# Kernel optimization log

Hardware: AMD Instinct MI355X
Metric: run time of the kernel (lower is better)

The kernel has to match this reference:

```python
import jax, jax.numpy as jnp
import numpy as np

N_NODES = 50000
N_EDGES = 1600000
NODE_DIM = 64
EDGE_DIM = 32
UNITS = 64


def _glorot(key, shape):
    fan_in, fan_out = shape[0], shape[1]
    lim = jnp.sqrt(6.0 / (fan_in + fan_out))
    return jax.random.uniform(key, shape, jnp.float32, -lim, lim)


def setup_inputs() -> dict:
    key = jax.random.key(0)
    ks = jax.random.split(key, 16)
    msg_in = 2 * NODE_DIM + EDGE_DIM  # concat(sender, receiver, edge)
    upd_in = NODE_DIM + UNITS         # concat(node, aggregated)
    return {
        "node_features": jax.random.normal(ks[0], (N_NODES, NODE_DIM), jnp.float32),
        "edge_features": jax.random.normal(ks[1], (N_EDGES, EDGE_DIM), jnp.float32),
        "senders": jax.random.randint(ks[2], (N_EDGES,), 0, N_NODES, jnp.int32),
        "receivers": jnp.sort(jax.random.randint(ks[3], (N_EDGES,), 0, N_NODES, jnp.int32)),
        # message_net
        "W1": _glorot(ks[4], (msg_in, UNITS)), "b1": jnp.zeros((UNITS,), jnp.float32),
        "W2": _glorot(ks[5], (UNITS, UNITS)), "b2": jnp.zeros((UNITS,), jnp.float32),
        # attention_net
        "Wa1": _glorot(ks[6], (msg_in, UNITS)), "ba1": jnp.zeros((UNITS,), jnp.float32),
        "Wa2": _glorot(ks[7], (UNITS, 1)), "ba2": jnp.zeros((1,), jnp.float32),
        # update_net
        "Wu1": _glorot(ks[8], (upd_in, UNITS)), "bu1": jnp.zeros((UNITS,), jnp.float32),
        "Wu2": _glorot(ks[9], (UNITS, UNITS)), "bu2": jnp.zeros((UNITS,), jnp.float32),
    }


def reference(node_features, edge_features, senders, receivers,
              W1, b1, W2, b2, Wa1, ba1, Wa2, ba2, Wu1, bu1, Wu2, bu2):
    act = jax.nn.swish
    # gather + concat: [E, 2*node_dim + edge_dim]
    msg_in = jnp.concatenate(
        [node_features[senders], node_features[receivers], edge_features], axis=-1)
    # message MLP
    messages = act(msg_in @ W1 + b1) @ W2 + b2  # [E, units]
    # attention: softmax over ALL edges (axis=0), as in the original
    att_logits = act(msg_in @ Wa1 + ba1) @ Wa2 + ba2  # [E, 1]
    att = jax.nn.softmax(att_logits, axis=0)
    messages = messages * att
    # scatter-sum to receivers
    aggregated = jax.ops.segment_sum(messages, receivers, num_segments=node_features.shape[0])
    upd_in = jnp.concatenate([node_features, aggregated], axis=-1)
    return act(upd_in @ Wu1 + bu1) @ Wu2 + bu2  # [N, units]
```

## Files before the change

### kernel.cpp

```cpp
#include <hip/hip_runtime.h>
#include <cstdint>
#include <cstddef>

#define N_NODES_C 50000
#define N_EDGES_C 1600000

typedef __attribute__((ext_vector_type(8)))  short bf16x8;
typedef __attribute__((ext_vector_type(16))) float f32x16;
typedef unsigned short ushort_t;

static const size_t AGG_OFF   = 256;
static const size_t NB_OFF    = 256 + (size_t)N_NODES_C * 64 * 4;
static const size_t WIMG_OFF  = NB_OFF + (size_t)N_NODES_C * 64 * 2;
static const size_t WUIMG_OFF = WIMG_OFF + 52224;

__device__ __forceinline__ float swish_(float v) { return v / (1.0f + __expf(-v)); }

__device__ __forceinline__ unsigned short f2bf(float f) {
    unsigned int u = __float_as_uint(f);
    return (unsigned short)((u + 0x7FFFu + ((u >> 16) & 1u)) >> 16);
}
__device__ __forceinline__ unsigned int pack2(float a, float b) {
    return (unsigned int)f2bf(a) | ((unsigned int)f2bf(b) << 16);
}

typedef __attribute__((address_space(3))) unsigned int lds_u32_t;
typedef const __attribute__((address_space(1))) unsigned int glb_u32_t;
__device__ __forceinline__ void glds16(const void* g, void* l) {
    __builtin_amdgcn_global_load_lds((glb_u32_t*)g, (lds_u32_t*)l, 16, 0, 0);
}

__global__ __launch_bounds__(256) void k_prep_node(const float* __restrict__ node,
                                                   ushort_t* __restrict__ node_bf)
{
    int i = blockIdx.x * 256 + threadIdx.x;
    if (i >= N_NODES_C * 64 / 8) return;
    const float4* s = (const float4*)node + (size_t)i * 2;
    float4 a = s[0], b = s[1];
    uint4 p = { pack2(a.x,a.y), pack2(a.z,a.w), pack2(b.x,b.y), pack2(b.z,b.w) };
    ((uint4*)node_bf)[i] = p;
}

__global__ __launch_bounds__(256) void k_prep_w(
    const float* __restrict__ W1, const float* __restrict__ Wa1,
    const float* __restrict__ W2, const float* __restrict__ Wu1,
    const float* __restrict__ Wu2,
    ushort_t* __restrict__ wm, ushort_t* __restrict__ wa, ushort_t* __restrict__ w2t,
    ushort_t* __restrict__ wu1t, ushort_t* __restrict__ wu2t)
{
    int b = blockIdx.x, t = threadIdx.x;
    const float* W; ushort_t* dst; int K, LP, p;
    if (b < 21)      { W = W1;  dst = wm;   K = 160; LP = 84; p = b * 256 + t; }
    else if (b < 42) { W = Wa1; dst = wa;   K = 160; LP = 84; p = (b-21)*256 + t; }
    else if (b < 51) { W = W2;  dst = w2t;  K = 64;  LP = 36; p = (b-42)*256 + t; }
    else if (b < 68) { W = Wu1; dst = wu1t; K = 128; LP = 68; p = (b-51)*256 + t; }
    else             { W = Wu2; dst = wu2t; K = 64;  LP = 36; p = (b-68)*256 + t; }
    int n = p / LP; int k2 = (p - n * LP) * 2;
    if (n >= 64) return;
    float a = (k2     < K) ? W[(size_t)k2 * 64 + n]       : 0.f;
    float c = (k2 + 1 < K) ? W[(size_t)(k2 + 1) * 64 + n] : 0.f;
    *(unsigned int*)(dst + (size_t)n * LP * 2 + k2) = pack2(a, c);
}

__global__ __launch_bounds__(512, 2) void k_edge(
    const ushort_t* __restrict__ node_bf, const float* __restrict__ edgef,
    const int* __restrict__ senders, const int* __restrict__ receivers,
    const ushort_t* __restrict__ wimg,
    const float* __restrict__ b1, const float* __restrict__ ba1,
    const float* __restrict__ Wa2, const float* __restrict__ ba2,
    const float* __restrict__ b2,
    float* __restrict__ expsum, float* __restrict__ agg)
{
    __shared__ ushort_t As[256 * 64];
    __shared__ ushort_t Ar[256 * 64];
    __shared__ ushort_t Ae[256 * 32];
    __shared__ ushort_t WmWa[21504];
    __shared__ ushort_t W2s[64 * 72];
    __shared__ float psum[8];

    const int tid = threadIdx.x;
    const int e0 = blockIdx.x * 256;

    for (int c = tid; c < 2688; c += 512)
        glds16((const char*)wimg + c * 16, (char*)WmWa + c * 16);
    for (int c = tid; c < 576; c += 512)
        glds16((const char*)wimg + 43008 + c * 16, (char*)W2s + c * 16);
    #pragma unroll
    for (int i = 0; i < 4; ++i) {
        int cg = tid + i * 512;
        int row = cg >> 3, c = cg & 7;
        glds16(node_bf + (size_t)senders[e0 + row] * 64 + ((c ^ (row & 7)) << 3),
               (char*)As + cg * 16);
    }
    #pragma unroll
    for (int i = 0; i < 4; ++i) {
        int cg = tid + i * 512;
        int row = cg >> 3, c = cg & 7;
        glds16(node_bf + (size_t)receivers[e0 + row] * 64 + ((c ^ (row & 7)) << 3),
               (char*)Ar + cg * 16);
    }
    {
        int row = tid >> 1, hf = tid & 1;
        const float4* ef = (const float4*)(edgef + (size_t)(e0 + row) * 32 + hf * 16);
        float4 x0 = ef[0], x1 = ef[1], x2 = ef[2], x3 = ef[3];
        uint4 p0 = { pack2(x0.x,x0.y), pack2(x0.z,x0.w), pack2(x1.x,x1.y), pack2(x1.z,x1.w) };
        uint4 p1 = { pack2(x2.x,x2.y), pack2(x2.z,x2.w), pack2(x3.x,x3.y), pack2(x3.z,x3.w) };
        int r3 = row & 3;
        *(uint4*)(Ae + row * 32 + (((2*hf)   ^ r3) << 3)) = p0;
        *(uint4*)(Ae + row * 32 + (((2*hf+1) ^ r3) << 3)) = p1;
    }
    __syncthreads();

    const int lane = tid & 63, w = tid >> 6;
    const int lr = lane & 31, hi = lane >> 5, kh = hi * 8;
    const int row_a = w * 32 + lr;
    const int r7 = lr & 7, r3 = lr & 3;

    f32x16 ca0, ca1, cm0, cm1;
    #pragma unroll
    for (int j = 0; j < 16; ++j) { ca0[j]=0.f; ca1[j]=0.f; cm0[j]=0.f; cm1[j]=0.f; }

    const ushort_t* asr = As + row_a * 64;
    const ushort_t* arr = Ar + row_a * 64;
    const ushort_t* aer = Ae + row_a * 32;
    const ushort_t* wm0 = WmWa + lr * 168 + kh;
    const ushort_t* wm1 = WmWa + (32 + lr) * 168 + kh;
    const ushort_t* wa0 = WmWa + 10752 + lr * 168 + kh;
    const ushort_t* wa1 = WmWa + 10752 + (32 + lr) * 168 + kh;

    #pragma unroll
    for (int kk = 0; kk < 4; ++kk) {
        bf16x8 a = *(const bf16x8*)(asr + (((2*kk + hi) ^ r7) << 3));
        cm0 = __builtin_amdgcn_mfma_f32_32x32x16_bf16(a, *(const bf16x8*)(wm0 + kk*16), cm0, 0,0,0);
        cm1 = __builtin_amdgcn_mfma_f32_32x32x16_bf16(a, *(const bf16x8*)(wm1 + kk*16), cm1, 0,0,0);
        ca0 = __builtin_amdgcn_mfma_f32_32x32x16_bf16(a, *(const bf16x8*)(wa0 + kk*16), ca0, 0,0,0);
        ca1 = __builtin_amdgcn_mfma_f32_32x32x16_bf16(a, *(const bf16x8*)(wa1 + kk*16), ca1, 0,0,0);
    }
    #pragma unroll
    for (int kk = 4; kk < 8; ++kk) {
        bf16x8 a = *(const bf16x8*)(arr + (((2*kk - 8 + hi) ^ r7) << 3));
        cm0 = __builtin_amdgcn_mfma_f32_32x32x16_bf16(a, *(const bf16x8*)(wm0 + kk*16), cm0, 0,0,0);
        cm1 = __builtin_amdgcn_mfma_f32_32x32x16_bf16(a, *(const bf16x8*)(wm1 + kk*16), cm1, 0,0,0);
        ca0 = __builtin_amdgcn_mfma_f32_32x32x16_bf16(a, *(const bf16x8*)(wa0 + kk*16), ca0, 0,0,0);
        ca1 = __builtin_amdgcn_mfma_f32_32x32x16_bf16(a, *(const bf16x8*)(wa1 + kk*16), ca1, 0,0,0);
    }
    #pragma unroll
    for (int kk = 8; kk < 10; ++kk) {
        bf16x8 a = *(const bf16x8*)(aer + (((2*kk - 16 + hi) ^ r3) << 3));
        cm0 = __builtin_amdgcn_mfma_f32_32x32x16_bf16(a, *(const bf16x8*)(wm0 + kk*16), cm0, 0,0,0);
        cm1 = __builtin_amdgcn_mfma_f32_32x32x16_bf16(a, *(const bf16x8*)(wm1 + kk*16), cm1, 0,0,0);
        ca0 = __builtin_amdgcn_mfma_f32_32x32x16_bf16(a, *(const bf16x8*)(wa0 + kk*16), ca0, 0,0,0);
        ca1 = __builtin_amdgcn_mfma_f32_32x32x16_bf16(a, *(const bf16x8*)(wa1 + kk*16), ca1, 0,0,0);
    }

    float p;
    {
        const float bb0 = ba1[lr], bb1 = ba1[32 + lr];
        const float wv0 = Wa2[lr], wv1 = Wa2[32 + lr];
        const float bb2 = ba2[0];
        float myl = 0.f;
        #pragma unroll
        for (int t = 0; t < 16; ++t) {
            float v = swish_(ca0[t] + bb0) * wv0 + swish_(ca1[t] + bb1) * wv1;
            v += __shfl_xor(v, 1);  v += __shfl_xor(v, 2);  v += __shfl_xor(v, 4);
            v += __shfl_xor(v, 8);  v += __shfl_xor(v, 16);
            if (lr == t) myl = v + bb2;
        }
        p = (lr < 16) ? __expf(myl) : 0.f;
        float ps = p;
        ps += __shfl_xor(ps, 1);  ps += __shfl_xor(ps, 2);  ps += __shfl_xor(ps, 4);
        ps += __shfl_xor(ps, 8);  ps += __shfl_xor(ps, 16); ps += __shfl_xor(ps, 32);
        if (lane == 0) psum[w] = ps;
    }
    __syncthreads();
    if (tid == 0) {
        float s = 0.f;
        #pragma unroll
        for (int q = 0; q < 8; ++q) s += psum[q];
        atomicAdd(expsum, s);
    }

    const float b10 = b1[lr], b11 = b1[32 + lr];
    ushort_t* H = WmWa;
    #pragma unroll
    for (int t = 0; t < 16; ++t) {
        int r = (t & 3) + 8 * (t >> 2) + 4 * hi;
        int g = (w * 32 + r) * 72;
        H[g + lr]      = f2bf(swish_(cm0[t] + b10));
        H[g + 32 + lr] = f2bf(swish_(cm1[t] + b11));
    }

    f32x16 d0, d1;
    #pragma unroll
    for (int j = 0; j < 16; ++j) { d0[j] = 0.f; d1[j] = 0.f; }
    const ushort_t* hp = H + row_a * 72 + kh;
    const ushort_t* q0 = W2s + lr * 72 + kh;
    const ushort_t* q1 = W2s + (32 + lr) * 72 + kh;
    #pragma unroll
    for (int kk = 0; kk < 4; ++kk) {
        bf16x8 a = *(const bf16x8*)(hp + kk * 16);
        d0 = __builtin_amdgcn_mfma_f32_32x32x16_bf16(a, *(const bf16x8*)(q0 + kk*16), d0, 0,0,0);
        d1 = __builtin_amdgcn_mfma_f32_32x32x16_bf16(a, *(const bf16x8*)(q1 + kk*16), d1, 0,0,0);
    }

    const float b20 = b2[lr], b21 = b2[32 + lr];
    float m0[16], m1[16];
    #pragma unroll
    for (int t = 0; t < 16; ++t) {
        int r = (t & 3) + 8 * (t >> 2) + 4 * hi;
        int src = ((r & 3) + 4 * (r >> 3)) + 32 * ((r >> 2) & 1);
        float wv = __shfl(p, src);
        m0[t] = (d0[t] + b20) * wv;
        m1[t] = (d1[t] + b21) * wv;
    }
    const int ews = e0 + w * 32;
    float acc = 0.f;
    int cur = receivers[ews];
    #pragma unroll
    for (int i = 0; i < 32; ++i) {
        int t = (i & 3) + 4 * (i >> 3);
        int sel = (i >> 2) & 1;
        float am = __shfl_xor(m0[t], 32);
        float bm = __shfl_xor(m1[t], 32);
        float low  = sel ? am : m0[t];
        float high = sel ? m1[t] : bm;
        float val = (lane < 32) ? low : high;
        int rr = receivers[ews + i];
        if (rr != cur) {
            atomicAdd(&agg[(size_t)cur * 64 + lane], acc);
            acc = 0.f; cur = rr;
        }
        acc += val;
    }
    atomicAdd(&agg[(size_t)cur * 64 + lane], acc);
}

__global__ __launch_bounds__(256) void k_upd(
    const ushort_t* __restrict__ node_bf, const float* __restrict__ agg,
    const ushort_t* __restrict__ wuimg,
    const float* __restrict__ bu1, const float* __restrict__ bu2,
    const float* __restrict__ expsum, float* __restrict__ out)
{
    __shared__ ushort_t Un[128 * 64];
    __shared__ ushort_t Ua[128 * 64];
    __shared__ ushort_t Wu[13312];
    __shared__ ushort_t H2[128 * 72];

    const int tid = threadIdx.x;
    const int n0 = blockIdx.x * 128;

    for (int c = tid; c < 1664; c += 256)
        glds16((const char*)wuimg + c * 16, (char*)Wu + c * 16);
    #pragma unroll
    for (int i = 0; i < 4; ++i) {
        int cg = tid + i * 256;
        int row = cg >> 3, c = cg & 7;
        int n = n0 + row; if (n >= N_NODES_C) n = N_NODES_C - 1;
        glds16(node_bf + (size_t)n * 64 + ((c ^ (row & 7)) << 3), (char*)Un + cg * 16);
    }
    const float invZ = 1.0f / expsum[0];
    {
        int row = tid >> 1, hf = tid & 1;
        int n = n0 + row; if (n >= N_NODES_C) n = N_NODES_C - 1;
        const float4* ap = (const float4*)(agg + (size_t)n * 64 + hf * 32);
        int r7 = row & 7;
        #pragma unroll
        for (int q = 0; q < 4; ++q) {
            float4 x = ap[2 * q], y = ap[2 * q + 1];
            uint4 pk = { pack2(x.x * invZ, x.y * invZ), pack2(x.z * invZ, x.w * invZ),
                         pack2(y.x * invZ, y.y * invZ), pack2(y.z * invZ, y.w * invZ) };
            int chunk = hf * 4 + q;
            *(uint4*)(Ua + row * 64 + ((chunk ^ r7) << 3)) = pk;
        }
    }
    __syncthreads();

    const int lane = tid & 63, w = tid >> 6;
    const int lr = lane & 31, hi = lane >> 5, kh = hi * 8;
    const int row_a = w * 32 + lr, r7 = lr & 7;

    f32x16 c0, c1;
    #pragma unroll
    for (int j = 0; j < 16; ++j) { c0[j] = 0.f; c1[j] = 0.f; }
    const ushort_t* un = Un + row_a * 64;
    const ushort_t* ua = Ua + row_a * 64;
    const ushort_t* w10 = Wu + lr * 136 + kh;
    const ushort_t* w11 = Wu + (32 + lr) * 136 + kh;
    #pragma unroll
    for (int kk = 0; kk < 4; ++kk) {
        bf16x8 a = *(const bf16x8*)(un + (((2*kk + hi) ^ r7) << 3));
        c0 = __builtin_amdgcn_mfma_f32_32x32x16_bf16(a, *(const bf16x8*)(w10 + kk*16), c0, 0,0,0);
        c1 = __builtin_amdgcn_mfma_f32_32x32x16_bf16(a, *(const bf16x8*)(w11 + kk*16), c1, 0,0,0);
    }
    #pragma unroll
    for (int kk = 4; kk < 8; ++kk) {
        bf16x8 a = *(const bf16x8*)(ua + (((2*kk - 8 + hi) ^ r7) << 3));
        c0 = __builtin_amdgcn_mfma_f32_32x32x16_bf16(a, *(const bf16x8*)(w10 + kk*16), c0, 0,0,0);
        c1 = __builtin_amdgcn_mfma_f32_32x32x16_bf16(a, *(const bf16x8*)(w11 + kk*16), c1, 0,0,0);
    }
    const float bb0 = bu1[lr], bb1 = bu1[32 + lr];
    #pragma unroll
    for (int t = 0; t < 16; ++t) {
        int r = (t & 3) + 8 * (t >> 2) + 4 * hi;
        int g = (w * 32 + r) * 72;
        H2[g + lr]      = f2bf(swish_(c0[t] + bb0));
        H2[g + 32 + lr] = f2bf(swish_(c1[t] + bb1));
    }
    f32x16 d0, d1;
    #pragma unroll
    for (int j = 0; j < 16; ++j) { d0[j] = 0.f; d1[j] = 0.f; }
    const ushort_t* hp = H2 + row_a * 72 + kh;
    const ushort_t* w20 = Wu + 8704 + lr * 72 + kh;
    const ushort_t* w21 = Wu + 8704 + (32 + lr) * 72 + kh;
    #pragma unroll
    for (int kk = 0; kk < 4; ++kk) {
        bf16x8 a = *(const bf16x8*)(hp + kk * 16);
        d0 = __builtin_amdgcn_mfma_f32_32x32x16_bf16(a, *(const bf16x8*)(w20 + kk*16), d0, 0,0,0);
        d1 = __builtin_amdgcn_mfma_f32_32x32x16_bf16(a, *(const bf16x8*)(w21 + kk*16), d1, 0,0,0);
    }
    const float ob0 = bu2[lr], ob1 = bu2[32 + lr];
    #pragma unroll
    for (int t = 0; t < 16; ++t) {
        int r = (t & 3) + 8 * (t >> 2) + 4 * hi;
        int g = n0 + w * 32 + r;
        if (g < N_NODES_C) {
            out[(size_t)g * 64 + lr]      = d0[t] + ob0;
            out[(size_t)g * 64 + 32 + lr] = d1[t] + ob1;
        }
    }
}

extern "C" void kernel_launch(void* const* d_in, const int* in_sizes, int n_in,
                              void* d_out, int out_size, void* d_ws, size_t ws_size,
                              hipStream_t stream)
{
    const float* node      = (const float*)d_in[0];
    const float* edgef     = (const float*)d_in[1];
    const int*   senders   = (const int*)d_in[2];
    const int*   receivers = (const int*)d_in[3];
    const float* W1  = (const float*)d_in[4];
    const float* b1  = (const float*)d_in[5];
    const float* W2  = (const float*)d_in[6];
    const float* b2  = (const float*)d_in[7];
    const float* Wa1 = (const float*)d_in[8];
    const float* ba1 = (const float*)d_in[9];
    const float* Wa2 = (const float*)d_in[10];
    const float* ba2 = (const float*)d_in[11];
    const float* Wu1 = (const float*)d_in[12];
    const float* bu1 = (const float*)d_in[13];
    const float* Wu2 = (const float*)d_in[14];
    const float* bu2 = (const float*)d_in[15];
    float* out = (float*)d_out;

    char* ws = (char*)d_ws;
    float*    expsum  = (float*)ws;
    float*    agg     = (float*)(ws + AGG_OFF);
    ushort_t* node_bf = (ushort_t*)(ws + NB_OFF);
    ushort_t* wimg    = (ushort_t*)(ws + WIMG_OFF);
    ushort_t* wuimg   = (ushort_t*)(ws + WUIMG_OFF);

    ushort_t* wm   = wimg;
    ushort_t* wa   = wimg + 10752;
    ushort_t* w2t  = wimg + 21504;
    ushort_t* wu1t = wuimg;
    ushort_t* wu2t = wuimg + 8704;

    hipMemsetAsync(ws, 0, AGG_OFF + (size_t)N_NODES_C * 64 * 4, stream);

    k_prep_node<<<(N_NODES_C * 64 / 8 + 255) / 256, 256, 0, stream>>>(node, node_bf);
    k_prep_w<<<77, 256, 0, stream>>>(W1, Wa1, W2, Wu1, Wu2, wm, wa, w2t, wu1t, wu2t);
    k_edge<<<N_EDGES_C / 256, 512, 0, stream>>>(node_bf, edgef, senders, receivers,
                                                wimg, b1, ba1, Wa2, ba2, b2, expsum, agg);
    k_upd<<<(N_NODES_C + 127) / 128, 256, 0, stream>>>(node_bf, agg, wuimg,
                                                       bu1, bu2, expsum, out);
}
```

Baseline: 629.0 us.

## Shrink edge tiles to 128, keep edge features in registers, compute attention logits with MFMA

The edge kernel now uses 128-edge blocks of 256 threads with a smaller shared-memory footprint (unpadded weight rows, XOR-swizzled W2) so more blocks fit per CU. Edge features go straight into registers instead of staging through LDS. Attention logits are reduced with an MFMA against a ones vector rather than shuffle trees. The global exp-sum atomic is spread across 8 slots to reduce contention, and messages pass through LDS for the segment scatter instead of cross-lane shuffles. This adds extra LDS round-trips and an extra MFMA stage, and weight loading is repeated across more blocks.

Measured after the change: 631.0 us. About the same (+0.3%).

```diff
diff --git a/kernel.cpp b/kernel.cpp
--- a/kernel.cpp
+++ b/kernel.cpp
@@ -9,10 +9,10 @@
 typedef __attribute__((ext_vector_type(16))) float f32x16;
 typedef unsigned short ushort_t;
 
-static const size_t AGG_OFF   = 256;
-static const size_t NB_OFF    = 256 + (size_t)N_NODES_C * 64 * 4;
+static const size_t AGG_OFF   = 512;
+static const size_t NB_OFF    = 512 + (size_t)N_NODES_C * 64 * 4;
 static const size_t WIMG_OFF  = NB_OFF + (size_t)N_NODES_C * 64 * 2;
-static const size_t WUIMG_OFF = WIMG_OFF + 52224;
+static const size_t WUIMG_OFF = WIMG_OFF + 49152;
 
 __device__ __forceinline__ float swish_(float v) { return v / (1.0f + __expf(-v)); }
 
@@ -22,6 +22,12 @@
 }
 __device__ __forceinline__ unsigned int pack2(float a, float b) {
     return (unsigned int)f2bf(a) | ((unsigned int)f2bf(b) << 16);
+}
+__device__ __forceinline__ bf16x8 pack8(float4 a, float4 b) {
+    union { uint4 u; bf16x8 v; } un;
+    un.u.x = pack2(a.x, a.y); un.u.y = pack2(a.z, a.w);
+    un.u.z = pack2(b.x, b.y); un.u.w = pack2(b.z, b.w);
+    return un.v;
 }
 
 typedef __attribute__((address_space(3))) unsigned int lds_u32_t;
@@ -45,24 +51,32 @@
     const float* __restrict__ W1, const float* __restrict__ Wa1,
     const float* __restrict__ W2, const float* __restrict__ Wu1,
     const float* __restrict__ Wu2,
-    ushort_t* __restrict__ wm, ushort_t* __restrict__ wa, ushort_t* __restrict__ w2t,
+    ushort_t* __restrict__ wm, ushort_t* __restrict__ wa, ushort_t* __restrict__ w2s,
     ushort_t* __restrict__ wu1t, ushort_t* __restrict__ wu2t)
 {
     int b = blockIdx.x, t = threadIdx.x;
-    const float* W; ushort_t* dst; int K, LP, p;
-    if (b < 21)      { W = W1;  dst = wm;   K = 160; LP = 84; p = b * 256 + t; }
-    else if (b < 42) { W = Wa1; dst = wa;   K = 160; LP = 84; p = (b-21)*256 + t; }
-    else if (b < 51) { W = W2;  dst = w2t;  K = 64;  LP = 36; p = (b-42)*256 + t; }
-    else if (b < 68) { W = Wu1; dst = wu1t; K = 128; LP = 68; p = (b-51)*256 + t; }
-    else             { W = Wu2; dst = wu2t; K = 64;  LP = 36; p = (b-68)*256 + t; }
-    int n = p / LP; int k2 = (p - n * LP) * 2;
-    if (n >= 64) return;
-    float a = (k2     < K) ? W[(size_t)k2 * 64 + n]       : 0.f;
-    float c = (k2 + 1 < K) ? W[(size_t)(k2 + 1) * 64 + n] : 0.f;
-    *(unsigned int*)(dst + (size_t)n * LP * 2 + k2) = pack2(a, c);
-}
-
-__global__ __launch_bounds__(512, 2) void k_edge(
+    if (b < 20) {
+        int p = b * 256 + t; int n = p / 80, j = p - n * 80;
+        ((unsigned int*)wm)[n * 80 + j] = pack2(W1[(size_t)(2*j) * 64 + n], W1[(size_t)(2*j+1) * 64 + n]);
+    } else if (b < 40) {
+        int p = (b - 20) * 256 + t; int n = p / 80, j = p - n * 80;
+        ((unsigned int*)wa)[n * 80 + j] = pack2(Wa1[(size_t)(2*j) * 64 + n], Wa1[(size_t)(2*j+1) * 64 + n]);
+    } else if (b < 48) {
+        int p = (b - 40) * 256 + t; int n = p >> 5, q = p & 31, c = q >> 2, j = q & 3;
+        ((unsigned int*)w2s)[n * 32 + ((c ^ (n & 7)) << 2) + j] =
+            pack2(W2[(size_t)(c*4 + j) * 64 + n], W2[(size_t)(c*4 + j + 32) * 64 + n]);
+    } else if (b < 65) {
+        int p = (b - 48) * 256 + t; int n = p / 68, j = p - n * 68; int k2 = 2 * j;
+        unsigned int v = (k2 < 128) ? pack2(Wu1[(size_t)k2 * 64 + n], Wu1[(size_t)(k2+1) * 64 + n]) : 0u;
+        ((unsigned int*)wu1t)[n * 68 + j] = v;
+    } else {
+        int p = (b - 65) * 256 + t; int n = p / 36, j = p - n * 36; int k2 = 2 * j;
+        unsigned int v = (k2 < 64) ? pack2(Wu2[(size_t)k2 * 64 + n], Wu2[(size_t)(k2+1) * 64 + n]) : 0u;
+        ((unsigned int*)wu2t)[n * 36 + j] = v;
+    }
+}
+
+__global__ __launch_bounds__(256, 2) void k_edge(
     const ushort_t* __restrict__ node_bf, const float* __restrict__ edgef,
     const int* __restrict__ senders, const int* __restrict__ receivers,
     const ushort_t* __restrict__ wimg,
@@ -71,66 +85,56 @@
     const float* __restrict__ b2,
     float* __restrict__ expsum, float* __restrict__ agg)
 {
-    __shared__ ushort_t As[256 * 64];
-    __shared__ ushort_t Ar[256 * 64];
-    __shared__ ushort_t Ae[256 * 32];
-    __shared__ ushort_t WmWa[21504];
-    __shared__ ushort_t W2s[64 * 72];
-    __shared__ float psum[8];
+    __shared__ ushort_t SMEM[40960];
+    ushort_t* As  = SMEM;
+    ushort_t* Ar  = SMEM + 8192;
+    ushort_t* Wm  = SMEM + 16384;
+    ushort_t* Wa  = SMEM + 26624;
+    ushort_t* W2s = SMEM + 36864;
 
     const int tid = threadIdx.x;
-    const int e0 = blockIdx.x * 256;
-
-    for (int c = tid; c < 2688; c += 512)
-        glds16((const char*)wimg + c * 16, (char*)WmWa + c * 16);
-    for (int c = tid; c < 576; c += 512)
-        glds16((const char*)wimg + 43008 + c * 16, (char*)W2s + c * 16);
+    const int e0 = blockIdx.x * 128;
+    const int lane = tid & 63, w = tid >> 6;
+    const int lr = lane & 31, hi = lane >> 5, kh = hi * 8;
+
+    for (int c = tid; c < 2560; c += 256)
+        glds16((const char*)wimg + c * 16, (char*)Wm + c * 16);
+    for (int c = tid; c < 512; c += 256)
+        glds16((const char*)wimg + 40960 + c * 16, (char*)W2s + c * 16);
     #pragma unroll
     for (int i = 0; i < 4; ++i) {
-        int cg = tid + i * 512;
+        int cg = tid + i * 256;
         int row = cg >> 3, c = cg & 7;
         glds16(node_bf + (size_t)senders[e0 + row] * 64 + ((c ^ (row & 7)) << 3),
                (char*)As + cg * 16);
     }
     #pragma unroll
     for (int i = 0; i < 4; ++i) {
-        int cg = tid + i * 512;
+        int cg = tid + i * 256;
         int row = cg >> 3, c = cg & 7;
         glds16(node_bf + (size_t)receivers[e0 + row] * 64 + ((c ^ (row & 7)) << 3),
                (char*)Ar + cg * 16);
     }
+    bf16x8 ae0, ae1;
     {
-        int row = tid >> 1, hf = tid & 1;
-        const float4* ef = (const float4*)(edgef + (size_t)(e0 + row) * 32 + hf * 16);
-        float4 x0 = ef[0], x1 = ef[1], x2 = ef[2], x3 = ef[3];
-        uint4 p0 = { pack2(x0.x,x0.y), pack2(x0.z,x0.w), pack2(x1.x,x1.y), pack2(x1.z,x1.w) };
-        uint4 p1 = { pack2(x2.x,x2.y), pack2(x2.z,x2.w), pack2(x3.x,x3.y), pack2(x3.z,x3.w) };
-        int r3 = row & 3;
-        *(uint4*)(Ae + row * 32 + (((2*hf)   ^ r3) << 3)) = p0;
-        *(uint4*)(Ae + row * 32 + (((2*hf+1) ^ r3) << 3)) = p1;
+        const float4* ep = (const float4*)(edgef + (size_t)(e0 + w * 32 + lr) * 32);
+        ae0 = pack8(ep[2 * hi], ep[2 * hi + 1]);
+        ae1 = pack8(ep[4 + 2 * hi], ep[4 + 2 * hi + 1]);
     }
     __syncthreads();
 
-    const int lane = tid & 63, w = tid >> 6;
-    const int lr = lane & 31, hi = lane >> 5, kh = hi * 8;
-    const int row_a = w * 32 + lr;
-    const int r7 = lr & 7, r3 = lr & 3;
-
     f32x16 ca0, ca1, cm0, cm1;
     #pragma unroll
     for (int j = 0; j < 16; ++j) { ca0[j]=0.f; ca1[j]=0.f; cm0[j]=0.f; cm1[j]=0.f; }
-
-    const ushort_t* asr = As + row_a * 64;
-    const ushort_t* arr = Ar + row_a * 64;
-    const ushort_t* aer = Ae + row_a * 32;
-    const ushort_t* wm0 = WmWa + lr * 168 + kh;
-    const ushort_t* wm1 = WmWa + (32 + lr) * 168 + kh;
-    const ushort_t* wa0 = WmWa + 10752 + lr * 168 + kh;
-    const ushort_t* wa1 = WmWa + 10752 + (32 + lr) * 168 + kh;
-
+    const ushort_t* asr = As + (w * 32 + lr) * 64;
+    const ushort_t* arr = Ar + (w * 32 + lr) * 64;
+    const ushort_t* wm0 = Wm + lr * 160 + kh;
+    const ushort_t* wm1 = Wm + (32 + lr) * 160 + kh;
+    const ushort_t* wa0 = Wa + lr * 160 + kh;
+    const ushort_t* wa1 = Wa + (32 + lr) * 160 + kh;
     #pragma unroll
     for (int kk = 0; kk < 4; ++kk) {
-        bf16x8 a = *(const bf16x8*)(asr + (((2*kk + hi) ^ r7) << 3));
+        bf16x8 a = *(const bf16x8*)(asr + (((2*kk + hi) ^ (lr & 7)) << 3));
         cm0 = __builtin_amdgcn_mfma_f32_32x32x16_bf16(a, *(const bf16x8*)(wm0 + kk*16), cm0, 0,0,0);
         cm1 = __builtin_amdgcn_mfma_f32_32x32x16_bf16(a, *(const bf16x8*)(wm1 + kk*16), cm1, 0,0,0);
         ca0 = __builtin_amdgcn_mfma_f32_32x32x16_bf16(a, *(const bf16x8*)(wa0 + kk*16), ca0, 0,0,0);
@@ -138,99 +142,95 @@
     }
     #pragma unroll
     for (int kk = 4; kk < 8; ++kk) {
-        bf16x8 a = *(const bf16x8*)(arr + (((2*kk - 8 + hi) ^ r7) << 3));
+        bf16x8 a = *(const bf16x8*)(arr + (((2*(kk-4) + hi) ^ (lr & 7)) << 3));
         cm0 = __builtin_amdgcn_mfma_f32_32x32x16_bf16(a, *(const bf16x8*)(wm0 + kk*16), cm0, 0,0,0);
         cm1 = __builtin_amdgcn_mfma_f32_32x32x16_bf16(a, *(const bf16x8*)(wm1 + kk*16), cm1, 0,0,0);
         ca0 = __builtin_amdgcn_mfma_f32_32x32x16_bf16(a, *(const bf16x8*)(wa0 + kk*16), ca0, 0,0,0);
         ca1 = __builtin_amdgcn_mfma_f32_32x32x16_bf16(a, *(const bf16x8*)(wa1 + kk*16), ca1, 0,0,0);
     }
-    #pragma unroll
-    for (int kk = 8; kk < 10; ++kk) {
-        bf16x8 a = *(const bf16x8*)(aer + (((2*kk - 16 + hi) ^ r3) << 3));
-        cm0 = __builtin_amdgcn_mfma_f32_32x32x16_bf16(a, *(const bf16x8*)(wm0 + kk*16), cm0, 0,0,0);
-        cm1 = __builtin_amdgcn_mfma_f32_32x32x16_bf16(a, *(const bf16x8*)(wm1 + kk*16), cm1, 0,0,0);
-        ca0 = __builtin_amdgcn_mfma_f32_32x32x16_bf16(a, *(const bf16x8*)(wa0 + kk*16), ca0, 0,0,0);
-        ca1 = __builtin_amdgcn_mfma_f32_32x32x16_bf16(a, *(const bf16x8*)(wa1 + kk*16), ca1, 0,0,0);
-    }
-
-    float p;
     {
-        const float bb0 = ba1[lr], bb1 = ba1[32 + lr];
-        const float wv0 = Wa2[lr], wv1 = Wa2[32 + lr];
-        const float bb2 = ba2[0];
-        float myl = 0.f;
-        #pragma unroll
-        for (int t = 0; t < 16; ++t) {
-            float v = swish_(ca0[t] + bb0) * wv0 + swish_(ca1[t] + bb1) * wv1;
-            v += __shfl_xor(v, 1);  v += __shfl_xor(v, 2);  v += __shfl_xor(v, 4);
-            v += __shfl_xor(v, 8);  v += __shfl_xor(v, 16);
-            if (lr == t) myl = v + bb2;
-        }
-        p = (lr < 16) ? __expf(myl) : 0.f;
-        float ps = p;
-        ps += __shfl_xor(ps, 1);  ps += __shfl_xor(ps, 2);  ps += __shfl_xor(ps, 4);
-        ps += __shfl_xor(ps, 8);  ps += __shfl_xor(ps, 16); ps += __shfl_xor(ps, 32);
-        if (lane == 0) psum[w] = ps;
+        bf16x8 a = ae0;
+        cm0 = __builtin_amdgcn_mfma_f32_32x32x16_bf16(a, *(const bf16x8*)(wm0 + 128), cm0, 0,0,0);
+        cm1 = __builtin_amdgcn_mfma_f32_32x32x16_bf16(a, *(const bf16x8*)(wm1 + 128), cm1, 0,0,0);
+        ca0 = __builtin_amdgcn_mfma_f32_32x32x16_bf16(a, *(const bf16x8*)(wa0 + 128), ca0, 0,0,0);
+        ca1 = __builtin_amdgcn_mfma_f32_32x32x16_bf16(a, *(const bf16x8*)(wa1 + 128), ca1, 0,0,0);
+        a = ae1;
+        cm0 = __builtin_amdgcn_mfma_f32_32x32x16_bf16(a, *(const bf16x8*)(wm0 + 144), cm0, 0,0,0);
+        cm1 = __builtin_amdgcn_mfma_f32_32x32x16_bf16(a, *(const bf16x8*)(wm1 + 144), cm1, 0,0,0);
+        ca0 = __builtin_amdgcn_mfma_f32_32x32x16_bf16(a, *(const bf16x8*)(wa0 + 144), ca0, 0,0,0);
+        ca1 = __builtin_amdgcn_mfma_f32_32x32x16_bf16(a, *(const bf16x8*)(wa1 + 144), ca1, 0,0,0);
     }
     __syncthreads();
-    if (tid == 0) {
-        float s = 0.f;
-        #pragma unroll
-        for (int q = 0; q < 8; ++q) s += psum[q];
-        atomicAdd(expsum, s);
-    }
+
+    ushort_t* H = Wa;
+    const float bb0 = ba1[lr], bb1 = ba1[32 + lr];
+    const float wv0 = Wa2[lr], wv1 = Wa2[32 + lr];
+    #pragma unroll
+    for (int t = 0; t < 16; ++t) {
+        int r = (t & 3) + 8 * (t >> 2) + 4 * hi;
+        *(unsigned int*)(H + (w * 32 + r) * 72 + 2 * lr) =
+            pack2(swish_(ca0[t] + bb0) * wv0, swish_(ca1[t] + bb1) * wv1);
+    }
+    f32x16 da;
+    #pragma unroll
+    for (int j = 0; j < 16; ++j) da[j] = 0.f;
+    bf16x8 ones;
+    #pragma unroll
+    for (int i = 0; i < 8; ++i) ones[i] = (short)0x3F80;
+    const ushort_t* hp = H + (w * 32 + lr) * 72 + kh;
+    #pragma unroll
+    for (int kk = 0; kk < 4; ++kk)
+        da = __builtin_amdgcn_mfma_f32_32x32x16_bf16(*(const bf16x8*)(hp + kk*16), ones, da, 0,0,0);
+
+    const float ba2v = ba2[0];
+    float p[16];
+    float ps = 0.f;
+    #pragma unroll
+    for (int t = 0; t < 16; ++t) { p[t] = __expf(da[t] + ba2v); ps += p[t]; }
+    ps += __shfl_xor(ps, 1);  ps += __shfl_xor(ps, 2);  ps += __shfl_xor(ps, 4);
+    ps += __shfl_xor(ps, 8);  ps += __shfl_xor(ps, 16); ps += __shfl_xor(ps, 32);
+    if (lane == 0) atomicAdd(&expsum[w * 16], ps * 0.03125f);
 
     const float b10 = b1[lr], b11 = b1[32 + lr];
-    ushort_t* H = WmWa;
-    #pragma unroll
-    for (int t = 0; t < 16; ++t) {
-        int r = (t & 3) + 8 * (t >> 2) + 4 * hi;
-        int g = (w * 32 + r) * 72;
-        H[g + lr]      = f2bf(swish_(cm0[t] + b10));
-        H[g + 32 + lr] = f2bf(swish_(cm1[t] + b11));
-    }
-
+    #pragma unroll
+    for (int t = 0; t < 16; ++t) {
+        int r = (t & 3) + 8 * (t >> 2) + 4 * hi;
+        *(unsigned int*)(H + (w * 32 + r) * 72 + 2 * lr) =
+            pack2(swish_(cm0[t] + b10), swish_(cm1[t] + b11));
+    }
     f32x16 d0, d1;
     #pragma unroll
     for (int j = 0; j < 16; ++j) { d0[j] = 0.f; d1[j] = 0.f; }
-    const ushort_t* hp = H + row_a * 72 + kh;
-    const ushort_t* q0 = W2s + lr * 72 + kh;
-    const ushort_t* q1 = W2s + (32 + lr) * 72 + kh;
+    const ushort_t* q0 = W2s + lr * 64;
+    const ushort_t* q1 = W2s + (32 + lr) * 64;
     #pragma unroll
     for (int kk = 0; kk < 4; ++kk) {
         bf16x8 a = *(const bf16x8*)(hp + kk * 16);
-        d0 = __builtin_amdgcn_mfma_f32_32x32x16_bf16(a, *(const bf16x8*)(q0 + kk*16), d0, 0,0,0);
-        d1 = __builtin_amdgcn_mfma_f32_32x32x16_bf16(a, *(const bf16x8*)(q1 + kk*16), d1, 0,0,0);
-    }
-
+        int sw = ((2*kk + hi) ^ (lr & 7)) << 3;
+        d0 = __builtin_amdgcn_mfma_f32_32x32x16_bf16(a, *(const bf16x8*)(q0 + sw), d0, 0,0,0);
+        d1 = __builtin_amdgcn_mfma_f32_32x32x16_bf16(a, *(const bf16x8*)(q1 + sw), d1, 0,0,0);
+    }
+
+    float* Msc = (float*)SMEM;
     const float b20 = b2[lr], b21 = b2[32 + lr];
-    float m0[16], m1[16];
-    #pragma unroll
-    for (int t = 0; t < 16; ++t) {
-        int r = (t & 3) + 8 * (t >> 2) + 4 * hi;
-        int src = ((r & 3) + 4 * (r >> 3)) + 32 * ((r >> 2) & 1);
-        float wv = __shfl(p, src);
-        m0[t] = (d0[t] + b20) * wv;
-        m1[t] = (d1[t] + b21) * wv;
-    }
+    #pragma unroll
+    for (int t = 0; t < 16; ++t) {
+        int r = (t & 3) + 8 * (t >> 2) + 4 * hi;
+        float2 mv = { (d0[t] + b20) * p[t], (d1[t] + b21) * p[t] };
+        *(float2*)(Msc + (w * 32 + r) * 64 + 2 * lr) = mv;
+    }
+    const int cj = (lane < 32) ? 2 * lane : 2 * (lane - 32) + 1;
     const int ews = e0 + w * 32;
     float acc = 0.f;
     int cur = receivers[ews];
-    #pragma unroll
+    #pragma unroll 4
     for (int i = 0; i < 32; ++i) {
-        int t = (i & 3) + 4 * (i >> 3);
-        int sel = (i >> 2) & 1;
-        float am = __shfl_xor(m0[t], 32);
-        float bm = __shfl_xor(m1[t], 32);
-        float low  = sel ? am : m0[t];
-        float high = sel ? m1[t] : bm;
-        float val = (lane < 32) ? low : high;
         int rr = receivers[ews + i];
         if (rr != cur) {
             atomicAdd(&agg[(size_t)cur * 64 + lane], acc);
             acc = 0.f; cur = rr;
         }
-        acc += val;
+        acc += Msc[(w * 32 + i) * 64 + cj];
     }
     atomicAdd(&agg[(size_t)cur * 64 + lane], acc);
 }
@@ -258,7 +258,10 @@
         int n = n0 + row; if (n >= N_NODES_C) n = N_NODES_C - 1;
         glds16(node_bf + (size_t)n * 64 + ((c ^ (row & 7)) << 3), (char*)Un + cg * 16);
     }
-    const float invZ = 1.0f / expsum[0];
+    float z = 0.f;
+    #pragma unroll
+    for (int q = 0; q < 8; ++q) z += expsum[q * 16];
+    const float invZ = 1.0f / z;
     {
         int row = tid >> 1, hf = tid & 1;
         int n = n0 + row; if (n >= N_NODES_C) n = N_NODES_C - 1;
@@ -294,7 +297,7 @@
     }
     #pragma unroll
     for (int kk = 4; kk < 8; ++kk) {
-        bf16x8 a = *(const bf16x8*)(ua + (((2*kk - 8 + hi) ^ r7) << 3));
+        bf16x8 a = *(const bf16x8*)(ua + (((2*(kk-4) + hi) ^ r7) << 3));
         c0 = __builtin_amdgcn_mfma_f32_32x32x16_bf16(a, *(const bf16x8*)(w10 + kk*16), c0, 0,0,0);
         c1 = __builtin_amdgcn_mfma_f32_32x32x16_bf16(a, *(const bf16x8*)(w11 + kk*16), c1, 0,0,0);
     }
@@ -360,16 +363,16 @@
     ushort_t* wuimg   = (ushort_t*)(ws + WUIMG_OFF);
 
     ushort_t* wm   = wimg;
-    ushort_t* wa   = wimg + 10752;
-    ushort_t* w2t  = wimg + 21504;
+    ushort_t* wa   = wimg + 10240;
+    ushort_t* w2s  = wimg + 20480;
     ushort_t* wu1t = wuimg;
     ushort_t* wu2t = wuimg + 8704;
 
     hipMemsetAsync(ws, 0, AGG_OFF + (size_t)N_NODES_C * 64 * 4, stream);
 
     k_prep_node<<<(N_NODES_C * 64 / 8 + 255) / 256, 256, 0, stream>>>(node, node_bf);
-    k_prep_w<<<77, 256, 0, stream>>>(W1, Wa1, W2, Wu1, Wu2, wm, wa, w2t, wu1t, wu2t);
-    k_edge<<<N_EDGES_C / 256, 512, 0, stream>>>(node_bf, edgef, senders, receivers,
+    k_prep_w<<<74, 256, 0, stream>>>(W1, Wa1, W2, Wu1, Wu2, wm, wa, w2s, wu1t, wu2t);
+    k_edge<<<N_EDGES_C / 128, 256, 0, stream>>>(node_bf, edgef, senders, receivers,
                                                 wimg, b1, ba1, Wa2, ba2, b2, expsum, agg);
     k_upd<<<(N_NODES_C + 127) / 128, 256, 0, stream>>>(node_bf, agg, wuimg,
                                                        bu1, bu2, expsum, out);
```
